# Optimization experiments

Hardware: AMD Instinct MI355X
Metric: run time of the kernel (lower is better)

## Reference

```python
import jax, jax.numpy as jnp
import numpy as np

B, S, D, H, L, F = 4, 2048, 512, 8, 4, 2048
DH = D // H
EPS = 1e-5


def setup_inputs() -> dict:
    key = jax.random.key(0)
    ks = jax.random.split(key, 16)
    sc = 0.02
    inp = {
        "turn_embeddings": jax.random.normal(ks[0], (B, S, D), jnp.float32),
        "Wqkv": jax.random.normal(ks[1], (L, 3 * D, D), jnp.float32) * sc,
        "bqkv": jnp.zeros((L, 3 * D), jnp.float32),
        "Wo": jax.random.normal(ks[2], (L, D, D), jnp.float32) * sc,
        "bo": jnp.zeros((L, D), jnp.float32),
        "W1": jax.random.normal(ks[3], (L, F, D), jnp.float32) * sc,
        "b1": jnp.zeros((L, F), jnp.float32),
        "W2": jax.random.normal(ks[4], (L, D, F), jnp.float32) * sc,
        "b2": jnp.zeros((L, D), jnp.float32),
        "ln1_g": jnp.ones((L, D), jnp.float32),
        "ln1_b": jnp.zeros((L, D), jnp.float32),
        "ln2_g": jnp.ones((L, D), jnp.float32),
        "ln2_b": jnp.zeros((L, D), jnp.float32),
        "speaker_ids": jax.random.randint(ks[5], (B, S), 0, 4, jnp.int64 if jax.config.jax_enable_x64 else jnp.int32),
    }
    return inp


def _layer_norm(x, g, b):
    mu = jnp.mean(x, axis=-1, keepdims=True)
    var = jnp.mean(jnp.square(x - mu), axis=-1, keepdims=True)
    return (x - mu) * jax.lax.rsqrt(var + EPS) * g + b


def _attention(x, Wqkv, bqkv, Wo, bo, allow):
    # x: [B,S,D]; allow: [B,1,S,S] boolean (causal & same-speaker)
    qkv = x @ Wqkv.T + bqkv                       # [B,S,3D]
    q, k, v = jnp.split(qkv, 3, axis=-1)
    q = q.reshape(x.shape[0], x.shape[1], H, DH)
    k = k.reshape(x.shape[0], x.shape[1], H, DH)
    v = v.reshape(x.shape[0], x.shape[1], H, DH)
    scores = jnp.einsum("bqhd,bkhd->bhqk", q, k) / np.sqrt(DH)
    scores = jnp.where(allow, scores, jnp.finfo(scores.dtype).min)
    p = jax.nn.softmax(scores, axis=-1)
    o = jnp.einsum("bhqk,bkhd->bqhd", p, v).reshape(x.shape[0], x.shape[1], D)
    return o @ Wo.T + bo


def reference(turn_embeddings, Wqkv, bqkv, Wo, bo, W1, b1, W2, b2,
              ln1_g, ln1_b, ln2_g, ln2_b, speaker_ids):
    Bc, Sc, _ = turn_embeddings.shape
    causal = jnp.tril(jnp.ones((Sc, Sc), bool))                 # [S,S]
    same = speaker_ids[:, :, None] == speaker_ids[:, None, :]    # [B,S,S]
    allow = (same & causal)[:, None, :, :]                       # [B,1,S,S]
    x = turn_embeddings
    for l in range(L):
        a = _attention(x, Wqkv[l], bqkv[l], Wo[l], bo[l], allow)
        x = _layer_norm(x + a, ln1_g[l], ln1_b[l])
        h = jax.nn.relu(x @ W1[l].T + b1[l]) @ W2[l].T + b2[l]
        x = _layer_norm(x + h, ln2_g[l], ln2_b[l])
    return x
```

## Files before the change

kernel.cpp:

```cpp
#include <hip/hip_runtime.h>
#include <stdint.h>

#define BN 4
#define SN 2048
#define DN 512
#define HN 8
#define LN 4
#define FN 2048
#define MN (BN * SN)
#define TD (3 * DN)

typedef __attribute__((ext_vector_type(8))) __bf16 bf16x8;
typedef __attribute__((ext_vector_type(4))) float f32x4;
typedef __attribute__((ext_vector_type(8))) unsigned short ushortx8;

static __device__ __forceinline__ unsigned short f2bf(float f) {
    return __builtin_bit_cast(unsigned short, (__bf16)f);
}
static __device__ __forceinline__ float bf2f(unsigned short h) {
    return __builtin_bit_cast(float, (uint32_t)h << 16);
}

static __device__ __forceinline__ void gload16(const void* g, void* l) {
    __builtin_amdgcn_global_load_lds(
        (const __attribute__((address_space(1))) void*)g,
        (__attribute__((address_space(3))) void*)l, 16, 0, 0);
}

__global__ __launch_bounds__(256) void k_cvt_all(const float* __restrict__ Wqkv,
                                                 const float* __restrict__ Wo,
                                                 const float* __restrict__ W1,
                                                 const float* __restrict__ W2,
                                                 const float* __restrict__ te,
                                                 unsigned short* __restrict__ wqkv_b,
                                                 unsigned short* __restrict__ wo_b,
                                                 unsigned short* __restrict__ w1_b,
                                                 unsigned short* __restrict__ w2_b,
                                                 unsigned short* __restrict__ xb) {
    constexpr int G0 = LN * TD * DN / 4;
    constexpr int G1 = G0 + LN * DN * DN / 4;
    constexpr int G2 = G1 + LN * FN * DN / 4;
    constexpr int G3 = G2 + LN * DN * FN / 4;
    constexpr int G4 = G3 + MN * DN / 4;
    int i = blockIdx.x * blockDim.x + threadIdx.x;
    int stride = gridDim.x * blockDim.x;
    for (; i < G4; i += stride) {
        const float* s; unsigned short* d; int j;
        if (i < G0)      { s = Wqkv; d = wqkv_b; j = i; }
        else if (i < G1) { s = Wo;   d = wo_b;   j = i - G0; }
        else if (i < G2) { s = W1;   d = w1_b;   j = i - G1; }
        else if (i < G3) { s = W2;   d = w2_b;   j = i - G2; }
        else             { s = te;   d = xb;     j = i - G3; }
        float4 v = ((const float4*)s)[j];
        ushort4 o;
        o.x = f2bf(v.x); o.y = f2bf(v.y); o.z = f2bf(v.z); o.w = f2bf(v.w);
        ((ushort4*)d)[j] = o;
    }
}

template <int MODE, int BNT>
__global__ __launch_bounds__(256) void k_gemm(const unsigned short* __restrict__ A,
                                              const unsigned short* __restrict__ B,
                                              const float* __restrict__ bias,
                                              unsigned short* __restrict__ Cb,
                                              int M, int N, int K, int GX) {
    __shared__ __align__(16) unsigned short As[2][128][32];
    __shared__ __align__(16) unsigned short Bs[2][BNT][32];
    constexpr int NFR = BNT / 32;
    constexpr int BCH = BNT / 16;

    const int t = threadIdx.x;
    const int lane = t & 63;
    const int wid = t >> 6;
    const int wm = wid >> 1, wn = wid & 1;
    const int lr = lane & 15;
    const int lg = lane >> 4;
    const int l3 = lr & 3;

    const int nwg = gridDim.x;
    const int bid = blockIdx.x;
    const int swz = (bid & 7) * (nwg >> 3) + (bid >> 3);
    const int bx = swz % GX;
    const int by = swz / GX;

    const size_t rowA = (size_t)by * 128;
    const size_t rowB = (size_t)bx * BNT;
    const unsigned short* Ab = A + rowA * K;
    const unsigned short* Bb = B + rowB * K;

    const int srow = lane >> 2;
    const int sgran = (lane & 3) ^ (srow & 3);

    f32x4 acc[4][NFR] = {};

    const int nit = K >> 5;

#pragma unroll
    for (int j = 0; j < 2; ++j) {
        const int c = wid * 2 + j;
        gload16(Ab + (size_t)(16 * c + srow) * K + sgran * 8, &As[0][16 * c][0]);
    }
#pragma unroll
    for (int j = 0; j < BCH / 4; ++j) {
        const int c = wid * (BCH / 4) + j;
        gload16(Bb + (size_t)(16 * c + srow) * K + sgran * 8, &Bs[0][16 * c][0]);
    }
    __syncthreads();

    for (int it = 0; it < nit; ++it) {
        const int cur = it & 1;
        if (it + 1 < nit) {
            const int k0 = (it + 1) << 5;
#pragma unroll
            for (int j = 0; j < 2; ++j) {
                const int c = wid * 2 + j;
                gload16(Ab + (size_t)(16 * c + srow) * K + k0 + sgran * 8,
                        &As[cur ^ 1][16 * c][0]);
            }
#pragma unroll
            for (int j = 0; j < BCH / 4; ++j) {
                const int c = wid * (BCH / 4) + j;
                gload16(Bb + (size_t)(16 * c + srow) * K + k0 + sgran * 8,
                        &Bs[cur ^ 1][16 * c][0]);
            }
        }

        const int gp = (lg ^ l3) * 8;
        bf16x8 af[4], bfr[NFR];
#pragma unroll
        for (int mi = 0; mi < 4; ++mi)
            af[mi] = *(const bf16x8*)&As[cur][wm * 64 + mi * 16 + lr][gp];
#pragma unroll
        for (int ni = 0; ni < NFR; ++ni)
            bfr[ni] = *(const bf16x8*)&Bs[cur][wn * (BNT / 2) + ni * 16 + lr][gp];
#pragma unroll
        for (int mi = 0; mi < 4; ++mi)
#pragma unroll
            for (int ni = 0; ni < NFR; ++ni)
                acc[mi][ni] = __builtin_amdgcn_mfma_f32_16x16x32_bf16(
                    af[mi], bfr[ni], acc[mi][ni], 0, 0, 0);

        __syncthreads();
    }

    float bv[NFR];
#pragma unroll
    for (int ni = 0; ni < NFR; ++ni)
        bv[ni] = bias[(int)rowB + wn * (BNT / 2) + ni * 16 + lr];

#pragma unroll
    for (int mi = 0; mi < 4; ++mi) {
#pragma unroll
        for (int ni = 0; ni < NFR; ++ni) {
            int col = (int)rowB + wn * (BNT / 2) + ni * 16 + lr;
            int row0 = (int)rowA + wm * 64 + mi * 16 + lg * 4;
#pragma unroll
            for (int r = 0; r < 4; ++r) {
                float v = acc[mi][ni][r] + bv[ni];
                if (MODE == 2) v = fmaxf(v, 0.f);
                Cb[(size_t)(row0 + r) * N + col] = f2bf(v);
            }
        }
    }
}

__global__ __launch_bounds__(256) void k_attn(const unsigned short* __restrict__ qkv,
                                              const int* __restrict__ spk,
                                              unsigned short* __restrict__ o) {
    __shared__ __align__(16) unsigned short Ks[2][64][64];
    __shared__ __align__(16) unsigned short Vt[2][64][64];
    __shared__ __align__(16) unsigned short Ps[4][16][64];

    const int t = threadIdx.x;
    const int lane = t & 63;
    const int w = t >> 6;
    const int lr = lane & 15;
    const int lg = lane >> 4;
    const int l7 = lr & 7;

    const int wg = blockIdx.x;
    const int inner = wg >> 3;
    const int bh = 4 * (wg & 7) + (inner & 3);
    const int qtile = (SN / 64 - 1) - (inner >> 2);
    const int b = bh >> 3;
    const int h = bh & 7;
    const int qb = qtile * 64;

    const size_t base = (size_t)b * SN * TD;
    const unsigned short* kg = qkv + base + DN + h * 64;
    const unsigned short* vg = qkv + base + 2 * DN + h * 64;

    const float SCL = 0.125f * 1.4426950408889634f;
    const unsigned short* qptr = qkv + base + (size_t)(qb + w * 16 + lr) * TD + h * 64;
    bf16x8 aq0 = *(const bf16x8*)(qptr + lg * 8);
    bf16x8 aq1 = *(const bf16x8*)(qptr + 32 + lg * 8);
#pragma unroll
    for (int j = 0; j < 8; ++j) {
        aq0[j] = (__bf16)((float)aq0[j] * SCL);
        aq1[j] = (__bf16)((float)aq1[j] * SCL);
    }

    int sqr[4], qrow[4];
#pragma unroll
    for (int r = 0; r < 4; ++r) {
        qrow[r] = qb + w * 16 + lg * 4 + r;
        sqr[r] = spk[b * SN + qrow[r]];
    }

    const int kr0 = t >> 3;
    const int kgr = ((t & 7) ^ (kr0 & 7)) * 8;
    const int vrow = t & 63;
    const int vd0 = (t >> 6) * 16;

    uint4 kra = *(const uint4*)&kg[(size_t)kr0 * TD + (t & 7) * 8];
    uint4 krb = *(const uint4*)&kg[(size_t)(kr0 + 32) * TD + (t & 7) * 8];
    ushortx8 vra = *(const ushortx8*)&vg[(size_t)vrow * TD + vd0];
    ushortx8 vrb = *(const ushortx8*)&vg[(size_t)vrow * TD + vd0 + 8];
    *(uint4*)&Ks[0][kr0][kgr] = kra;
    *(uint4*)&Ks[0][kr0 + 32][kgr] = krb;
#pragma unroll
    for (int j = 0; j < 8; ++j) {
        const int vc0 = (((vrow >> 3) ^ j) << 3) + (vrow & 7);
        Vt[0][vd0 + j][vc0] = vra[j];
        Vt[0][vd0 + 8 + j][vc0] = vrb[j];
    }

    float lsum[4] = {0.f, 0.f, 0.f, 0.f};
    f32x4 acc_o[4] = {};

    const int ntiles = qtile + 1;
    for (int it = 0; it < ntiles; ++it) {
        const int k0 = it * 64;
        const int cur = it & 1;
        __syncthreads();

        const bool nx = (it + 1 < ntiles);
        if (nx) {
            const int kn = k0 + 64;
            kra = *(const uint4*)&kg[(size_t)(kn + kr0) * TD + (t & 7) * 8];
            krb = *(const uint4*)&kg[(size_t)(kn + kr0 + 32) * TD + (t & 7) * 8];
            vra = *(const ushortx8*)&vg[(size_t)(kn + vrow) * TD + vd0];
            vrb = *(const ushortx8*)&vg[(size_t)(kn + vrow) * TD + vd0 + 8];
        }
        int skr[4];
#pragma unroll
        for (int ni = 0; ni < 4; ++ni) skr[ni] = spk[b * SN + k0 + 16 * ni + lr];

        f32x4 sc4[4] = {};
        __builtin_amdgcn_s_setprio(1);
#pragma unroll
        for (int ni = 0; ni < 4; ++ni) {
            bf16x8 bk0 = *(const bf16x8*)&Ks[cur][16 * ni + lr][(lg ^ l7) * 8];
            bf16x8 bk1 = *(const bf16x8*)&Ks[cur][16 * ni + lr][((lg + 4) ^ l7) * 8];
            sc4[ni] = __builtin_amdgcn_mfma_f32_16x16x32_bf16(aq0, bk0, sc4[ni], 0, 0, 0);
            sc4[ni] = __builtin_amdgcn_mfma_f32_16x16x32_bf16(aq1, bk1, sc4[ni], 0, 0, 0);
        }
        __builtin_amdgcn_s_setprio(0);

        const bool diag = (it == ntiles - 1);
#pragma unroll
        for (int ni = 0; ni < 4; ++ni) {
#pragma unroll
            for (int r = 0; r < 4; ++r) {
                bool allow = (skr[ni] == sqr[r]);
                if (diag) allow = allow && (16 * ni + lr <= w * 16 + lg * 4 + r);
                float p = allow ? __builtin_amdgcn_exp2f(sc4[ni][r]) : 0.f;
                lsum[r] += p;
                const int q7 = (lg * 4 + r) & 7;
                const int pg = ((2 * ni + (lr >> 3)) ^ q7) * 8 + l7;
                Ps[w][lg * 4 + r][pg] = f2bf(p);
            }
        }

        bf16x8 ap0 = *(const bf16x8*)&Ps[w][lr][(lg ^ l7) * 8];
        bf16x8 ap1 = *(const bf16x8*)&Ps[w][lr][((lg + 4) ^ l7) * 8];
        __builtin_amdgcn_s_setprio(1);
#pragma unroll
        for (int ni = 0; ni < 4; ++ni) {
            bf16x8 bv0 = *(const bf16x8*)&Vt[cur][16 * ni + lr][(lg ^ l7) * 8];
            bf16x8 bv1 = *(const bf16x8*)&Vt[cur][16 * ni + lr][((lg + 4) ^ l7) * 8];
            acc_o[ni] = __builtin_amdgcn_mfma_f32_16x16x32_bf16(ap0, bv0, acc_o[ni], 0, 0, 0);
            acc_o[ni] = __builtin_amdgcn_mfma_f32_16x16x32_bf16(ap1, bv1, acc_o[ni], 0, 0, 0);
        }
        __builtin_amdgcn_s_setprio(0);

        if (nx) {
            const int nb = cur ^ 1;
            *(uint4*)&Ks[nb][kr0][kgr] = kra;
            *(uint4*)&Ks[nb][kr0 + 32][kgr] = krb;
#pragma unroll
            for (int j = 0; j < 8; ++j) {
                const int vc0 = (((vrow >> 3) ^ j) << 3) + (vrow & 7);
                Vt[nb][vd0 + j][vc0] = vra[j];
                Vt[nb][vd0 + 8 + j][vc0] = vrb[j];
            }
        }
    }

#pragma unroll
    for (int r = 0; r < 4; ++r) {
        float s = lsum[r];
        s += __shfl_xor(s, 1);
        s += __shfl_xor(s, 2);
        s += __shfl_xor(s, 4);
        s += __shfl_xor(s, 8);
        float inv = 1.f / s;
#pragma unroll
        for (int ni = 0; ni < 4; ++ni) {
            int d = 16 * ni + lr;
            o[(size_t)(b * SN + qrow[r]) * DN + h * 64 + d] = f2bf(acc_o[ni][r] * inv);
        }
    }
}

template <bool XF32>
__global__ __launch_bounds__(256) void k_add_ln(const void* __restrict__ xin_,
                                                const unsigned short* __restrict__ dl,
                                                const float* __restrict__ g,
                                                const float* __restrict__ bta,
                                                unsigned short* __restrict__ xb,
                                                float* __restrict__ fout) {
    const int row = blockIdx.x * 4 + (threadIdx.x >> 6);
    const int lane = threadIdx.x & 63;
    const size_t off = (size_t)row * DN + lane * 8;
    const int c0 = lane * 8;

    float v[8];
    if (XF32) {
        const float* xin = (const float*)xin_;
        float4 a0 = *(const float4*)&xin[off];
        float4 a1 = *(const float4*)&xin[off + 4];
        v[0] = a0.x; v[1] = a0.y; v[2] = a0.z; v[3] = a0.w;
        v[4] = a1.x; v[5] = a1.y; v[6] = a1.z; v[7] = a1.w;
    } else {
        ushortx8 xa = *(const ushortx8*)&((const unsigned short*)xin_)[off];
#pragma unroll
        for (int i = 0; i < 8; ++i) v[i] = bf2f(xa[i]);
    }
    ushortx8 dd = *(const ushortx8*)&dl[off];
#pragma unroll
    for (int i = 0; i < 8; ++i) v[i] += bf2f(dd[i]);

    float s1 = 0.f, s2 = 0.f;
#pragma unroll
    for (int i = 0; i < 8; ++i) { s1 += v[i]; s2 += v[i] * v[i]; }
#pragma unroll
    for (int msk = 32; msk; msk >>= 1) {
        s1 += __shfl_xor(s1, msk);
        s2 += __shfl_xor(s2, msk);
    }
    const float mean = s1 * (1.f / 512.f);
    const float var = s2 * (1.f / 512.f) - mean * mean;
    const float rs = rsqrtf(var + 1e-5f);

    float4 g0 = *(const float4*)&g[c0];
    float4 g1 = *(const float4*)&g[c0 + 4];
    float4 b0 = *(const float4*)&bta[c0];
    float4 b1 = *(const float4*)&bta[c0 + 4];
    float gg[8] = {g0.x, g0.y, g0.z, g0.w, g1.x, g1.y, g1.z, g1.w};
    float bb[8] = {b0.x, b0.y, b0.z, b0.w, b1.x, b1.y, b1.z, b1.w};

    float y[8];
    ushortx8 ub;
#pragma unroll
    for (int i = 0; i < 8; ++i) {
        y[i] = (v[i] - mean) * rs * gg[i] + bb[i];
        ub[i] = f2bf(y[i]);
    }
    *(ushortx8*)&xb[off] = ub;
    if (fout) {
        *(float4*)&fout[off] = make_float4(y[0], y[1], y[2], y[3]);
        *(float4*)&fout[off + 4] = make_float4(y[4], y[5], y[6], y[7]);
    }
}

extern "C" void kernel_launch(void* const* d_in, const int* in_sizes, int n_in,
                              void* d_out, int out_size, void* d_ws, size_t ws_size,
                              hipStream_t stream) {
    const float* te   = (const float*)d_in[0];
    const float* Wqkv = (const float*)d_in[1];
    const float* bqkv = (const float*)d_in[2];
    const float* Wo   = (const float*)d_in[3];
    const float* bo   = (const float*)d_in[4];
    const float* W1   = (const float*)d_in[5];
    const float* b1   = (const float*)d_in[6];
    const float* W2   = (const float*)d_in[7];
    const float* b2   = (const float*)d_in[8];
    const float* g1   = (const float*)d_in[9];
    const float* be1  = (const float*)d_in[10];
    const float* g2   = (const float*)d_in[11];
    const float* be2  = (const float*)d_in[12];
    const int*   spk  = (const int*)d_in[13];
    float* out = (float*)d_out;

    char* ws = (char*)d_ws;
    size_t off = 0;
    auto alloc = [&](size_t bytes) -> char* {
        char* p = ws + off;
        off += (bytes + 255) & ~(size_t)255;
        return p;
    };
    unsigned short* wqkv_b = (unsigned short*)alloc((size_t)LN * TD * DN * 2);
    unsigned short* wo_b   = (unsigned short*)alloc((size_t)LN * DN * DN * 2);
    unsigned short* w1_b   = (unsigned short*)alloc((size_t)LN * FN * DN * 2);
    unsigned short* w2_b   = (unsigned short*)alloc((size_t)LN * DN * FN * 2);
    unsigned short* xb     = (unsigned short*)alloc((size_t)MN * DN * 2);
    unsigned short* u      = (unsigned short*)alloc((size_t)MN * FN * 2);
    unsigned short* ob     = (unsigned short*)alloc((size_t)MN * DN * 2);
    unsigned short* projb  = (unsigned short*)alloc((size_t)MN * DN * 2);
    unsigned short* qkvb = u;
    unsigned short* hb   = u;

    k_cvt_all<<<2048, 256, 0, stream>>>(Wqkv, Wo, W1, W2, te,
                                        wqkv_b, wo_b, w1_b, w2_b, xb);

    for (int l = 0; l < LN; ++l) {
        k_gemm<1, 128><<<(MN / 128) * (TD / 128), 256, 0, stream>>>(
            xb, wqkv_b + (size_t)l * TD * DN, bqkv + l * TD, qkvb,
            MN, TD, DN, TD / 128);
        k_attn<<<(SN / 64) * BN * HN, 256, 0, stream>>>(qkvb, spk, ob);
        k_gemm<1, 64><<<(MN / 128) * (DN / 64), 256, 0, stream>>>(
            ob, wo_b + (size_t)l * DN * DN, bo + l * DN, projb,
            MN, DN, DN, DN / 64);
        if (l == 0)
            k_add_ln<true><<<MN / 4, 256, 0, stream>>>(
                te, projb, g1 + l * DN, be1 + l * DN, xb, nullptr);
        else
            k_add_ln<false><<<MN / 4, 256, 0, stream>>>(
                xb, projb, g1 + l * DN, be1 + l * DN, xb, nullptr);
        k_gemm<2, 128><<<(MN / 128) * (FN / 128), 256, 0, stream>>>(
            xb, w1_b + (size_t)l * FN * DN, b1 + l * FN, hb,
            MN, FN, DN, FN / 128);
        k_gemm<1, 64><<<(MN / 128) * (DN / 64), 256, 0, stream>>>(
            hb, w2_b + (size_t)l * DN * FN, b2 + l * DN, projb,
            MN, DN, FN, DN / 64);
        k_add_ln<false><<<MN / 4, 256, 0, stream>>>(
            xb, projb, g2 + l * DN, be2 + l * DN, xb,
            (l == LN - 1) ? out : nullptr);
    }
    (void)in_sizes; (void)n_in; (void)out_size; (void)ws_size;
}
```

Measured before the change: 637.2 us.

## Overlap GEMM prefetch with compute via partial vmcnt waits and new LDS swizzle

The GEMM main loop replaces the full __syncthreads at the top of each stage with an explicit s_waitcnt on only the current buffer's loads, so the next stage's global-to-LDS loads can stay in flight while MFMAs run. The LDS XOR swizzle changes to use (row>>1)&3 so that fragment reads hit fewer bank conflicts, and address arithmetic is hoisted into a precomputed offset. The hard-coded vmcnt counts depend on how many loads each wave issues, so a change in tile size or in the compiler's load ordering could break correctness.

```diff
diff --git a/kernel.cpp b/kernel.cpp
--- a/kernel.cpp
+++ b/kernel.cpp
@@ -67,7 +67,7 @@
     __shared__ __align__(16) unsigned short As[2][128][32];
     __shared__ __align__(16) unsigned short Bs[2][BNT][32];
     constexpr int NFR = BNT / 32;
-    constexpr int BCH = BNT / 16;
+    constexpr int BCHW = BNT / 64;
 
     const int t = threadIdx.x;
     const int lane = t & 63;
@@ -75,7 +75,6 @@
     const int wm = wid >> 1, wn = wid & 1;
     const int lr = lane & 15;
     const int lg = lane >> 4;
-    const int l3 = lr & 3;
 
     const int nwg = gridDim.x;
     const int bid = blockIdx.x;
@@ -89,23 +88,22 @@
     const unsigned short* Bb = B + rowB * K;
 
     const int srow = lane >> 2;
-    const int sgran = (lane & 3) ^ (srow & 3);
+    const int sgran = (lane & 3) ^ ((srow >> 1) & 3);
+    const size_t soff = (size_t)srow * K + sgran * 8;
 
     f32x4 acc[4][NFR] = {};
-
     const int nit = K >> 5;
 
 #pragma unroll
     for (int j = 0; j < 2; ++j) {
         const int c = wid * 2 + j;
-        gload16(Ab + (size_t)(16 * c + srow) * K + sgran * 8, &As[0][16 * c][0]);
-    }
-#pragma unroll
-    for (int j = 0; j < BCH / 4; ++j) {
-        const int c = wid * (BCH / 4) + j;
-        gload16(Bb + (size_t)(16 * c + srow) * K + sgran * 8, &Bs[0][16 * c][0]);
-    }
-    __syncthreads();
+        gload16(Ab + (size_t)(16 * c) * K + soff, &As[0][16 * c][0]);
+    }
+#pragma unroll
+    for (int j = 0; j < BCHW; ++j) {
+        const int c = wid * BCHW + j;
+        gload16(Bb + (size_t)(16 * c) * K + soff, &Bs[0][16 * c][0]);
+    }
 
     for (int it = 0; it < nit; ++it) {
         const int cur = it & 1;
@@ -114,18 +112,21 @@
 #pragma unroll
             for (int j = 0; j < 2; ++j) {
                 const int c = wid * 2 + j;
-                gload16(Ab + (size_t)(16 * c + srow) * K + k0 + sgran * 8,
-                        &As[cur ^ 1][16 * c][0]);
+                gload16(Ab + (size_t)(16 * c) * K + k0 + soff, &As[cur ^ 1][16 * c][0]);
             }
 #pragma unroll
-            for (int j = 0; j < BCH / 4; ++j) {
-                const int c = wid * (BCH / 4) + j;
-                gload16(Bb + (size_t)(16 * c + srow) * K + k0 + sgran * 8,
-                        &Bs[cur ^ 1][16 * c][0]);
+            for (int j = 0; j < BCHW; ++j) {
+                const int c = wid * BCHW + j;
+                gload16(Bb + (size_t)(16 * c) * K + k0 + soff, &Bs[cur ^ 1][16 * c][0]);
             }
-        }
-
-        const int gp = (lg ^ l3) * 8;
+            if (BNT == 128) asm volatile("s_waitcnt vmcnt(4)" ::: "memory");
+            else            asm volatile("s_waitcnt vmcnt(3)" ::: "memory");
+        } else {
+            asm volatile("s_waitcnt vmcnt(0)" ::: "memory");
+        }
+        __builtin_amdgcn_s_barrier();
+
+        const int gp = (lg ^ ((lr >> 1) & 3)) * 8;
         bf16x8 af[4], bfr[NFR];
 #pragma unroll
         for (int mi = 0; mi < 4; ++mi)
@@ -140,7 +141,7 @@
                 acc[mi][ni] = __builtin_amdgcn_mfma_f32_16x16x32_bf16(
                     af[mi], bfr[ni], acc[mi][ni], 0, 0, 0);
 
-        __syncthreads();
+        __builtin_amdgcn_s_barrier();
     }
 
     float bv[NFR];
```

New measurement: 624.1 us. 2.1% less time.
